# Kernel optimization log

Measured on AMD Instinct MI355X. Metric: run time of the kernel, lower is better.

Reference implementation:

```python
import jax, jax.numpy as jnp
import numpy as np

N = 16384

def setup_inputs() -> dict:
    key = jax.random.key(0)
    k1, k2 = jax.random.split(key)
    predict = jax.random.normal(k1, (N,), dtype=jnp.float32)
    target = jax.random.normal(k2, (N,), dtype=jnp.float32)
    return {"predict": predict, "target": target}

def reference(predict, target):
    n = predict.shape[0]
    # hardtanh(predict[i]-predict[j]) * hardtanh(target[i]-target[j]) summed over i>j.
    # The product matrix is symmetric with zero diagonal, so the strict lower-
    # triangular sum equals half the full-matrix sum.
    pd = jnp.clip(predict[:, None] - predict[None, :], -1.0, 1.0)  # [N, N]
    td = jnp.clip(target[:, None] - target[None, :], -1.0, 1.0)   # [N, N]
    full_sum = jnp.sum(pd * td)
    num = full_sum * 0.5
    denom = jnp.asarray(n * (n - 1), dtype=predict.dtype)
    return 1.0 - 2.0 * num / denom
```

## Files before the change

kernel.cpp:

```cpp
#include <hip/hip_runtime.h>

#define BLOCK 512
#define IPT   4
#define ITILE 2048
#define JS    128
#define JT_PER_I 16
#define NT    576

typedef _Float16 h2 __attribute__((ext_vector_type(2)));

__global__ __launch_bounds__(BLOCK) void kendall_fused(
    const float* __restrict__ p, const float* __restrict__ t,
    float* __restrict__ partial, unsigned int* __restrict__ cnt,
    float* __restrict__ out, int n) {
    __shared__ unsigned int sjp[JS / 2];
    __shared__ unsigned int sjt[JS / 2];
    __shared__ float wsum[BLOCK / 64];
    __shared__ int lastFlag;

    const int s = blockIdx.x;
    int bi = (int)((__builtin_sqrtf(4.0f + 2.0f * (float)s) - 2.0f) * 0.25f);
    while (8 * (bi + 1) * (bi + 2) <= s) ++bi;
    while (8 * bi * (bi + 1) > s) --bi;
    const int bj = s - 8 * bi * (bi + 1);
    const float w = (bj < JT_PER_I * bi) ? 2.0f : 1.0f;

    if (threadIdx.x < JS) {
        const int k = threadIdx.x & 63;
        const float2* src = (const float2*)((threadIdx.x < 64 ? p : t) + bj * JS);
        float2 v = src[k];
        h2 hv = {(_Float16)v.x, (_Float16)v.y};
        unsigned int bitsv; __builtin_memcpy(&bitsv, &hv, 4);
        (threadIdx.x < 64 ? sjp : sjt)[k] = bitsv;
    }

    h2 pi2[IPT], ti2[IPT];
#pragma unroll
    for (int u = 0; u < IPT; ++u) {
        int i = bi * ITILE + u * BLOCK + threadIdx.x;
        _Float16 ph = (_Float16)p[i];
        _Float16 th = (_Float16)t[i];
        pi2[u] = (h2){ph, ph};
        ti2[u] = (h2){th, th};
    }
    __syncthreads();

    const h2 neg1 = {(_Float16)-1.0f, (_Float16)-1.0f};
    const h2 pos1 = {(_Float16)1.0f, (_Float16)1.0f};

    float acc[IPT] = {0.0f};
    const uint4* jp4 = (const uint4*)sjp;
    const uint4* jt4 = (const uint4*)sjt;

#pragma unroll 4
    for (int g = 0; g < JS / 8; ++g) {
        uint4 jp = jp4[g];
        uint4 jt = jt4[g];
        unsigned int jpw[4] = {jp.x, jp.y, jp.z, jp.w};
        unsigned int jtw[4] = {jt.x, jt.y, jt.z, jt.w};
#pragma unroll
        for (int c = 0; c < 4; ++c) {
            h2 pj, tj;
            __builtin_memcpy(&pj, &jpw[c], 4);
            __builtin_memcpy(&tj, &jtw[c], 4);
#pragma unroll
            for (int u = 0; u < IPT; ++u) {
                h2 pd = __builtin_elementwise_min(
                            __builtin_elementwise_max(pi2[u] - pj, neg1), pos1);
                h2 td = __builtin_elementwise_min(
                            __builtin_elementwise_max(ti2[u] - tj, neg1), pos1);
                acc[u] = __builtin_amdgcn_fdot2(pd, td, acc[u], false);
            }
        }
    }

    float r = (acc[0] + acc[1]) + (acc[2] + acc[3]);
#pragma unroll
    for (int off = 32; off > 0; off >>= 1) r += __shfl_down(r, off, 64);

    if ((threadIdx.x & 63) == 0) wsum[threadIdx.x >> 6] = r;
    __syncthreads();

    if (threadIdx.x == 0) {
        float b = 0.0f;
#pragma unroll
        for (int v2 = 0; v2 < BLOCK / 64; ++v2) b += wsum[v2];
        partial[s] = w * b;
        __threadfence();
        unsigned int old = atomicAdd(cnt, 1u);
        lastFlag = (old == NT - 1);
    }
    __syncthreads();

    if (lastFlag) {
        float v = 0.0f;
        const volatile float* vp = partial;
        for (int k = threadIdx.x; k < NT; k += BLOCK) v += vp[k];
#pragma unroll
        for (int off = 32; off > 0; off >>= 1) v += __shfl_down(v, off, 64);
        if ((threadIdx.x & 63) == 0) wsum[threadIdx.x >> 6] = v;
        __syncthreads();
        if (threadIdx.x == 0) {
            float S = 0.0f;
#pragma unroll
            for (int v2 = 0; v2 < BLOCK / 64; ++v2) S += wsum[v2];
            float denom = (float)n * (float)(n - 1);
            out[0] = 1.0f - S / denom;
        }
    }
}

extern "C" void kernel_launch(void* const* d_in, const int* in_sizes, int n_in,
                              void* d_out, int out_size, void* d_ws, size_t ws_size,
                              hipStream_t stream) {
    const float* predict = (const float*)d_in[0];
    const float* target  = (const float*)d_in[1];
    float* out = (float*)d_out;
    float* partial = (float*)d_ws;
    unsigned int* cnt = (unsigned int*)d_ws + NT;
    const int n = in_sizes[0];

    hipMemsetAsync(cnt, 0, sizeof(unsigned int), stream);
    kendall_fused<<<NT, BLOCK, 0, stream>>>(predict, target, partial, cnt, out, n);
}
```

Measured before the change: 79.30 us.

## Replace atomic last-block reduction with cooperative grid sync and vectorize i loads

Drops the memset and the atomic-counter last-block pattern. A cooperative launch now uses a grid-wide sync, after which block 0 sums the partials. It also loads each thread's four i values with one float4 load instead of four strided scalar loads, which changes which i elements each thread owns but not the total. Cooperative launch adds grid-sync overhead and needs all 576 blocks of 512 threads to be resident at once, or the launch fails.

```diff
diff --git a/kernel.cpp b/kernel.cpp
--- a/kernel.cpp
+++ b/kernel.cpp
@@ -1,4 +1,7 @@
 #include <hip/hip_runtime.h>
+#include <hip/hip_cooperative_groups.h>
+
+namespace cg = cooperative_groups;
 
 #define BLOCK 512
 #define IPT   4
@@ -9,14 +12,12 @@
 
 typedef _Float16 h2 __attribute__((ext_vector_type(2)));
 
-__global__ __launch_bounds__(BLOCK) void kendall_fused(
+__global__ __launch_bounds__(BLOCK) void kendall_coop(
     const float* __restrict__ p, const float* __restrict__ t,
-    float* __restrict__ partial, unsigned int* __restrict__ cnt,
-    float* __restrict__ out, int n) {
+    float* __restrict__ partial, float* __restrict__ out, int n) {
     __shared__ unsigned int sjp[JS / 2];
     __shared__ unsigned int sjt[JS / 2];
     __shared__ float wsum[BLOCK / 64];
-    __shared__ int lastFlag;
 
     const int s = blockIdx.x;
     int bi = (int)((__builtin_sqrtf(4.0f + 2.0f * (float)s) - 2.0f) * 0.25f);
@@ -34,14 +35,19 @@
         (threadIdx.x < 64 ? sjp : sjt)[k] = bitsv;
     }
 
+    const int ibase = bi * ITILE + 4 * threadIdx.x;
+    float4 pv = *(const float4*)(p + ibase);
+    float4 tv = *(const float4*)(t + ibase);
     h2 pi2[IPT], ti2[IPT];
-#pragma unroll
-    for (int u = 0; u < IPT; ++u) {
-        int i = bi * ITILE + u * BLOCK + threadIdx.x;
-        _Float16 ph = (_Float16)p[i];
-        _Float16 th = (_Float16)t[i];
-        pi2[u] = (h2){ph, ph};
-        ti2[u] = (h2){th, th};
+    {
+        _Float16 a0 = (_Float16)pv.x, a1 = (_Float16)pv.y,
+                 a2 = (_Float16)pv.z, a3 = (_Float16)pv.w;
+        pi2[0] = (h2){a0, a0}; pi2[1] = (h2){a1, a1};
+        pi2[2] = (h2){a2, a2}; pi2[3] = (h2){a3, a3};
+        _Float16 b0 = (_Float16)tv.x, b1 = (_Float16)tv.y,
+                 b2 = (_Float16)tv.z, b3 = (_Float16)tv.w;
+        ti2[0] = (h2){b0, b0}; ti2[1] = (h2){b1, b1};
+        ti2[2] = (h2){b2, b2}; ti2[3] = (h2){b3, b3};
     }
     __syncthreads();
 
@@ -80,22 +86,18 @@
 
     if ((threadIdx.x & 63) == 0) wsum[threadIdx.x >> 6] = r;
     __syncthreads();
-
     if (threadIdx.x == 0) {
         float b = 0.0f;
 #pragma unroll
         for (int v2 = 0; v2 < BLOCK / 64; ++v2) b += wsum[v2];
         partial[s] = w * b;
-        __threadfence();
-        unsigned int old = atomicAdd(cnt, 1u);
-        lastFlag = (old == NT - 1);
     }
-    __syncthreads();
 
-    if (lastFlag) {
+    cg::this_grid().sync();
+
+    if (blockIdx.x == 0) {
         float v = 0.0f;
-        const volatile float* vp = partial;
-        for (int k = threadIdx.x; k < NT; k += BLOCK) v += vp[k];
+        for (int k = threadIdx.x; k < NT; k += BLOCK) v += partial[k];
 #pragma unroll
         for (int off = 32; off > 0; off >>= 1) v += __shfl_down(v, off, 64);
         if ((threadIdx.x & 63) == 0) wsum[threadIdx.x >> 6] = v;
@@ -117,9 +119,10 @@
     const float* target  = (const float*)d_in[1];
     float* out = (float*)d_out;
     float* partial = (float*)d_ws;
-    unsigned int* cnt = (unsigned int*)d_ws + NT;
-    const int n = in_sizes[0];
+    int n = in_sizes[0];
 
-    hipMemsetAsync(cnt, 0, sizeof(unsigned int), stream);
-    kendall_fused<<<NT, BLOCK, 0, stream>>>(predict, target, partial, cnt, out, n);
+    void* args[] = {(void*)&predict, (void*)&target, (void*)&partial,
+                    (void*)&out, (void*)&n};
+    hipLaunchCooperativeKernel((const void*)kendall_coop, dim3(NT), dim3(BLOCK),
+                               args, 0, stream);
 }
```

Result: slower. 113.0 us (+42.4%).
